# Performance work log

Hardware: AMD Instinct MI355X
Metric: run time of the kernel (lower is better)

Reference implementation:

```python
import jax, jax.numpy as jnp
import numpy as np

B, SQ, SK, D, UNITS = 4, 2048, 2048, 1024, 1024

def setup_inputs() -> dict:
    key = jax.random.key(0)
    ks = jax.random.split(key, 5)
    scale = 1.0 / np.sqrt(D)
    return {
        "q": jax.random.normal(ks[0], (B, SQ, D), dtype=jnp.float32),
        "k": jax.random.normal(ks[1], (B, SK, D), dtype=jnp.float32),
        "v": jax.random.normal(ks[2], (B, SK, D), dtype=jnp.float32),
        "W1_w": jax.random.normal(ks[3], (D, UNITS), dtype=jnp.float32) * scale,
        "W1_b": jnp.zeros((UNITS,), dtype=jnp.float32),
        "W2_w": jax.random.normal(ks[4], (D, UNITS), dtype=jnp.float32) * scale,
        "W2_b": jnp.zeros((UNITS,), dtype=jnp.float32),
    }

def reference(q, k, v, W1_w, W1_b, W2_w, W2_b):
    # Dense projections (keras Dense: x @ W + b)
    l1 = q @ W1_w + W1_b            # [B, Sq, units]
    l2 = k @ W2_w + W2_b            # [B, Sk, units]
    # score = l1 @ l2^T, scaled by sqrt(score.shape[2]) == sqrt(Sk) (as in original)
    inv_scale = 1.0 / np.sqrt(k.shape[1]).astype(np.float32)
    score = jnp.einsum('bqu,bku->bqk', l1, l2) * inv_scale  # [B, Sq, Sk]
    dist = jax.nn.softmax(score, axis=-1)
    att = jnp.einsum('bqk,bkd->bqd', dist, v)               # [B, Sq, d_v]
    return att
```

## Files before the change

### kernel.cpp

```cpp
#include <hip/hip_runtime.h>
#include <cmath>
#include <stdint.h>


typedef short short8 __attribute__((ext_vector_type(8)));
typedef float f32x4 __attribute__((ext_vector_type(4)));
typedef __bf16 bf16x8 __attribute__((ext_vector_type(8)));
typedef unsigned int u32x4 __attribute__((ext_vector_type(4)));

typedef __attribute__((address_space(3))) void lds_void;
typedef __attribute__((address_space(1))) void gbl_void;

__device__ __forceinline__ unsigned short f2b(float x) {
    unsigned u = __builtin_bit_cast(unsigned, x);
    u += 0x7fffu + ((u >> 16) & 1u);
    return (unsigned short)(u >> 16);
}

__global__ void prep_kernel(const float* __restrict__ v,
                            const float* __restrict__ W1,
                            const float* __restrict__ W2,
                            unsigned short* __restrict__ vT,
                            unsigned short* __restrict__ W1t,
                            unsigned short* __restrict__ W2t,
                            float* __restrict__ rs) {
    const int bz = blockIdx.z;
    const int t = threadIdx.x;
    const int tid2 = blockIdx.y * 64 + blockIdx.x;

    if (bz == 4 && tid2 >= 256 && tid2 < 288) {
        if (rs) rs[(tid2 - 256) * 256 + t] = 0.f;
        return;
    }

    __shared__ float tile[64][65];
    const float* in;
    unsigned short* out;
    int R, C;
    if (bz < 4) {
        R = 2048; C = 1024;
        in = v + (long)bz * R * C;
        out = vT + (long)bz * R * C;
    } else {
        R = 1024; C = 1024;
        if (tid2 >= 256) return;
        in = (bz == 4) ? W1 : W2;
        out = (bz == 4) ? W1t : W2t;
    }
    const int rt = (tid2 >> 4) * 64;
    const int ct = (tid2 & 15) * 64;

    {
        const int rr = t >> 2;
        const int cb = (t & 3) * 16;
        const float* src = in + (long)(rt + rr) * C + ct + cb;
#pragma unroll
        for (int u = 0; u < 4; u++) {
            float4 a = *(const float4*)(src + 4 * u);
            tile[rr][cb + 4 * u + 0] = a.x;
            tile[rr][cb + 4 * u + 1] = a.y;
            tile[rr][cb + 4 * u + 2] = a.z;
            tile[rr][cb + 4 * u + 3] = a.w;
        }
    }
    __syncthreads();
    {
        const int cc = t >> 2;
        const int rb = (t & 3) * 16;
        unsigned short* dst = out + (long)(ct + cc) * R + rt + rb;
#pragma unroll
        for (int u = 0; u < 2; u++) {
            union { short8 v8; unsigned short us[8]; } o;
#pragma unroll
            for (int e = 0; e < 8; e++) o.us[e] = f2b(tile[rb + 8 * u + e][cc]);
            *(short8*)(dst + 8 * u) = o.v8;
        }
    }
}

__device__ __forceinline__ void load16_to_lds(const unsigned short* g,
                                              unsigned short* l) {
    __builtin_amdgcn_global_load_lds((gbl_void*)g, (lds_void*)l, 16, 0, 0);
}

template <int MODE, int CASTA>
__global__ __launch_bounds__(512, 4) void gemm256_kernel(
                               const unsigned short* __restrict__ A,
                               const unsigned short* __restrict__ Bt,
                               const float* __restrict__ bias0,
                               const float* __restrict__ bias1,
                               float* __restrict__ rowsum,
                               void* __restrict__ Cout,
                               int M, int N, int K,
                               float scale,
                               long sA, long sB, long sC,
                               const float* __restrict__ Afq,
                               const float* __restrict__ Afk) {
    __shared__ __align__(16) unsigned short As[256 * 64];
    __shared__ __align__(16) unsigned short Bs[128 * 64];

    int bx, by, bz;
    {
        const int nx = gridDim.x;
        const int Rt = gridDim.y * gridDim.z;
        if ((Rt & 7) == 0) {
            int flat = ((int)blockIdx.z * gridDim.y + blockIdx.y) * nx + blockIdx.x;
            int rpx = Rt >> 3;
            int c = flat & 7;
            int j = flat >> 3;
            bx = j / rpx;
            int yg = c * rpx + (j - bx * rpx);
            bz = yg / gridDim.y;
            by = yg - bz * gridDim.y;
        } else {
            bx = blockIdx.x; by = blockIdx.y; bz = blockIdx.z;
        }
    }

    Bt += (long)bz * sB;

    const int t = threadIdx.x;
    const int lane = t & 63;
    const int wave = t >> 6;
    const int wm = wave >> 1, wn = wave & 1;
    const int row0 = by * 256;
    const int col0 = bx * 128;

    const int rS = lane >> 3;
    const int kOffS = ((lane & 7) ^ rS) * 8;
    const unsigned short* gA[4];
    const float* fA[4];
    unsigned short* lA[4];
    const unsigned short* gB[2];
    unsigned short* lB[2];
#pragma unroll
    for (int i = 0; i < 4; i++) {
        const int rowl = wave * 32 + i * 8;
        lA[i] = As + rowl * 64;
        if (CASTA) {
            const float* Af = bz ? Afk : Afq;
            fA[i] = Af + (long)(row0 + rowl + rS) * K + kOffS;
        } else {
            gA[i] = A + (long)bz * sA + (long)(row0 + rowl + rS) * K + kOffS;
        }
    }
#pragma unroll
    for (int i = 0; i < 2; i++) {
        const int rowl = wave * 16 + i * 8;
        gB[i] = Bt + (long)(col0 + rowl + rS) * K + kOffS;
        lB[i] = Bs + rowl * 64;
    }

    const int lr = lane & 15;
    const int quad = lane >> 4;
    const int pc0 = (quad ^ (lr & 7)) * 8;
    const int pc1 = ((4 + quad) ^ (lr & 7)) * 8;

    f32x4 acc[4][4];
#pragma unroll
    for (int i = 0; i < 4; i++)
#pragma unroll
        for (int j = 0; j < 4; j++) acc[i][j] = f32x4{0.f, 0.f, 0.f, 0.f};

    for (int k0 = 0; k0 < K; k0 += 64) {
#pragma unroll
        for (int i = 0; i < 2; i++) load16_to_lds(gB[i] + k0, lB[i]);
        if (CASTA) {
#pragma unroll
            for (int i = 0; i < 4; i++) {
                const float* s = fA[i] + k0;
                float4 x = *(const float4*)(s);
                float4 y = *(const float4*)(s + 4);
                unsigned w0, w1, w2, w3;
                asm("v_cvt_pk_bf16_f32 %0, %1, %2" : "=v"(w0) : "v"(x.x), "v"(x.y));
                asm("v_cvt_pk_bf16_f32 %0, %1, %2" : "=v"(w1) : "v"(x.z), "v"(x.w));
                asm("v_cvt_pk_bf16_f32 %0, %1, %2" : "=v"(w2) : "v"(y.x), "v"(y.y));
                asm("v_cvt_pk_bf16_f32 %0, %1, %2" : "=v"(w3) : "v"(y.z), "v"(y.w));
                *(u32x4*)(lA[i] + lane * 8) = u32x4{w0, w1, w2, w3};
            }
        } else {
#pragma unroll
            for (int i = 0; i < 4; i++) load16_to_lds(gA[i] + k0, lA[i]);
        }
        __syncthreads();

#pragma unroll
        for (int ks = 0; ks < 2; ks++) {
            const int pc = ks ? pc1 : pc0;
            bf16x8 a[4], b[4];
#pragma unroll
            for (int i = 0; i < 4; i++) {
                a[i] = __builtin_bit_cast(bf16x8,
                    *(const short8*)(As + (wm * 64 + i * 16 + lr) * 64 + pc));
                b[i] = __builtin_bit_cast(bf16x8,
                    *(const short8*)(Bs + (wn * 64 + i * 16 + lr) * 64 + pc));
            }
#pragma unroll
            for (int i = 0; i < 4; i++)
#pragma unroll
                for (int j = 0; j < 4; j++)
                    acc[i][j] = __builtin_amdgcn_mfma_f32_16x16x32_bf16(
                        a[i], b[j], acc[i][j], 0, 0, 0);
        }
        __syncthreads();
    }

    const long cbase = (long)bz * sC;

    if (MODE == 0) {
        const float* bp = (bz && bias1) ? bias1 : bias0;
#pragma unroll
        for (int j = 0; j < 4; j++) {
            const int gcol = col0 + wn * 64 + j * 16 + lr;
            const float bv = bp[gcol];
#pragma unroll
            for (int i = 0; i < 4; i++) {
                const int growb = row0 + wm * 64 + i * 16 + quad * 4;
#pragma unroll
                for (int r = 0; r < 4; r++) {
                    float val = acc[i][j][r] * scale + bv;
                    ((unsigned short*)Cout)[cbase + (long)(growb + r) * N + gcol] = f2b(val);
                }
            }
        }
    } else {
        float psum[4][4];
#pragma unroll
        for (int i = 0; i < 4; i++)
#pragma unroll
            for (int r = 0; r < 4; r++) psum[i][r] = 0.f;
#pragma unroll
        for (int j = 0; j < 4; j++) {
            const int gcol = col0 + wn * 64 + j * 16 + lr;
#pragma unroll
            for (int i = 0; i < 4; i++) {
                const int growb = row0 + wm * 64 + i * 16 + quad * 4;
#pragma unroll
                for (int r = 0; r < 4; r++) {
                    float e = __expf(acc[i][j][r] * scale);
                    psum[i][r] += e;
                    ((unsigned short*)Cout)[cbase + (long)(growb + r) * N + gcol] = f2b(e);
                }
            }
        }
#pragma unroll
        for (int i = 0; i < 4; i++)
#pragma unroll
            for (int r = 0; r < 4; r++) {
                float s = psum[i][r];
                s += __shfl_xor(s, 1);
                s += __shfl_xor(s, 2);
                s += __shfl_xor(s, 4);
                s += __shfl_xor(s, 8);
                if (lr == 0) {
                    const int grow = row0 + wm * 64 + i * 16 + quad * 4 + r;
                    atomicAdd(rowsum + (long)bz * M + grow, s);
                }
            }
    }
}

template <int MODE>
__global__ void gemm128_kernel(const unsigned short* __restrict__ A,
                               const unsigned short* __restrict__ Bt,
                               const float* __restrict__ bias0,
                               const float* __restrict__ bias1,
                               float* __restrict__ rowsum,
                               void* __restrict__ Cout,
                               int M, int N, int K,
                               float scale,
                               long sA, long sB, long sC) {
    __shared__ __align__(16) unsigned short As[128 * 64];
    __shared__ __align__(16) unsigned short Bs[128 * 64];

    int bx, by, bz;
    {
        const int nx = gridDim.x;
        const int Rt = gridDim.y * gridDim.z;
        if ((Rt & 7) == 0) {
            int flat = ((int)blockIdx.z * gridDim.y + blockIdx.y) * nx + blockIdx.x;
            int rpx = Rt >> 3;
            int c = flat & 7;
            int j = flat >> 3;
            bx = j / rpx;
            int yg = c * rpx + (j - bx * rpx);
            bz = yg / gridDim.y;
            by = yg - bz * gridDim.y;
        } else {
            bx = blockIdx.x; by = blockIdx.y; bz = blockIdx.z;
        }
    }

    A  += (long)bz * sA;
    Bt += (long)bz * sB;

    const int t = threadIdx.x;
    const int lane = t & 63;
    const int wave = t >> 6;
    const int wm = wave >> 1, wn = wave & 1;
    const int row0 = by * 128;
    const int col0 = bx * 128;

    const int rS = lane >> 3;
    const int kOffS = ((lane & 7) ^ rS) * 8;
    const unsigned short* gA[4];
    const unsigned short* gB[4];
    unsigned short* lA[4];
    unsigned short* lB[4];
#pragma unroll
    for (int i = 0; i < 4; i++) {
        const int rowl = i * 32 + wave * 8 + rS;
        const int ldsrow = i * 32 + wave * 8;
        gA[i] = A  + (long)(row0 + rowl) * K + kOffS;
        gB[i] = Bt + (long)(col0 + rowl) * K + kOffS;
        lA[i] = As + ldsrow * 64;
        lB[i] = Bs + ldsrow * 64;
    }

    const int lr = lane & 15;
    const int quad = lane >> 4;
    const int pc0 = (quad ^ (lr & 7)) * 8;
    const int pc1 = ((4 + quad) ^ (lr & 7)) * 8;

    f32x4 acc[4][4];
#pragma unroll
    for (int i = 0; i < 4; i++)
#pragma unroll
        for (int j = 0; j < 4; j++) acc[i][j] = f32x4{0.f, 0.f, 0.f, 0.f};

    for (int k0 = 0; k0 < K; k0 += 64) {
#pragma unroll
        for (int i = 0; i < 4; i++) {
            load16_to_lds(gA[i] + k0, lA[i]);
            load16_to_lds(gB[i] + k0, lB[i]);
        }
        __syncthreads();

#pragma unroll
        for (int ks = 0; ks < 2; ks++) {
            const int pc = ks ? pc1 : pc0;
            bf16x8 a[4], b[4];
#pragma unroll
            for (int i = 0; i < 4; i++) {
                a[i] = __builtin_bit_cast(bf16x8,
                    *(const short8*)(As + (wm * 64 + i * 16 + lr) * 64 + pc));
                b[i] = __builtin_bit_cast(bf16x8,
                    *(const short8*)(Bs + (wn * 64 + i * 16 + lr) * 64 + pc));
            }
#pragma unroll
            for (int i = 0; i < 4; i++)
#pragma unroll
                for (int j = 0; j < 4; j++)
                    acc[i][j] = __builtin_amdgcn_mfma_f32_16x16x32_bf16(
                        a[i], b[j], acc[i][j], 0, 0, 0);
        }
        __syncthreads();
    }

    const long cbase = (long)bz * sC;

    if (MODE == 2) {
#pragma unroll
        for (int i = 0; i < 4; i++) {
            const int growb = row0 + wm * 64 + i * 16 + quad * 4;
#pragma unroll
            for (int r = 0; r < 4; r++) {
                const float inv = 1.0f / rowsum[(long)bz * M + growb + r];
#pragma unroll
                for (int j = 0; j < 4; j++) {
                    const int gcol = col0 + wn * 64 + j * 16 + lr;
                    ((float*)Cout)[cbase + (long)(growb + r) * N + gcol] =
                        acc[i][j][r] * inv;
                }
            }
        }
    }
}

extern "C" void kernel_launch(void* const* d_in, const int* in_sizes, int n_in,
                              void* d_out, int out_size, void* d_ws, size_t ws_size,
                              hipStream_t stream) {
    const float* q   = (const float*)d_in[0];
    const float* k   = (const float*)d_in[1];
    const float* v   = (const float*)d_in[2];
    const float* W1w = (const float*)d_in[3];
    const float* W1b = (const float*)d_in[4];
    const float* W2w = (const float*)d_in[5];
    const float* W2b = (const float*)d_in[6];
    float* out = (float*)d_out;

    const int B = 4, SQ = 2048, SK = 2048, D = 1024, U = 1024;
    char* ws = (char*)d_ws;
    const size_t MB = 1024 * 1024;
    unsigned short* vT  = (unsigned short*)(ws + 32 * MB);
    unsigned short* W1t = (unsigned short*)(ws + 48 * MB);
    unsigned short* W2t = (unsigned short*)(ws + 50 * MB);
    unsigned short* l1  = (unsigned short*)(ws + 52 * MB);
    unsigned short* l2  = (unsigned short*)(ws + 68 * MB);
    unsigned short* sc  = (unsigned short*)(ws + 0);

    float* rowsum;
    bool prep_zeroes_rowsum;
    if (ws_size >= 85 * MB) {
        rowsum = (float*)(ws + 84 * MB);
        prep_zeroes_rowsum = true;
    } else {
        rowsum = (float*)(ws + 50 * MB);
        prep_zeroes_rowsum = false;
    }

    prep_kernel<<<dim3(64, 8, 6), 256, 0, stream>>>(
        v, W1w, W2w, vT, W1t, W2t,
        prep_zeroes_rowsum ? rowsum : nullptr);
    gemm256_kernel<0, 1><<<dim3(U / 128, (B * SQ) / 256, 2), 512, 0, stream>>>(
        nullptr, W1t, W1b, W2b, nullptr, l1, B * SQ, U, D, 1.0f,
        0, (long)1024 * 1024, (long)8 * 1024 * 1024, q, k);
    if (!prep_zeroes_rowsum)
        hipMemsetAsync(rowsum, 0, (size_t)B * SQ * sizeof(float), stream);
    const float invs = 1.0f / sqrtf((float)SK);
    gemm256_kernel<1, 0><<<dim3(SK / 128, SQ / 256, B), 512, 0, stream>>>(
        l1, l2, nullptr, nullptr, rowsum, sc, SQ, SK, U, invs,
        (long)SQ * U, (long)SK * U, (long)SQ * SK, nullptr, nullptr);
    gemm128_kernel<2><<<dim3(D / 128, SQ / 128, B), 256, 0, stream>>>(
        sc, vT, nullptr, nullptr, rowsum, out, SQ, D, SK, 1.0f,
        (long)SQ * SK, (long)D * SK, (long)SQ * D);
}
```

Baseline: 261.7 us.

## Pre-cast q/k to bf16 in prep and fold V transpose into score GEMM

The fp32-to-bf16 conversion of q and k moves out of the projection GEMM's inner loop into the prep kernel, so the projection GEMM can stream both operands with async global_load_lds. The V transpose-and-cast leaves the prep kernel and runs as extra blocks (bz >= 4) of the score GEMM launch, so it overlaps with score tiles instead of running as a separate pass. The trade-off is extra HBM traffic for the bf16 copies of q and k, and the transpose blocks now compete with GEMM blocks for the CUs.

```diff
diff --git a/kernel.cpp b/kernel.cpp
--- a/kernel.cpp
+++ b/kernel.cpp
@@ -6,7 +6,6 @@
 typedef short short8 __attribute__((ext_vector_type(8)));
 typedef float f32x4 __attribute__((ext_vector_type(4)));
 typedef __bf16 bf16x8 __attribute__((ext_vector_type(8)));
-typedef unsigned int u32x4 __attribute__((ext_vector_type(4)));
 
 typedef __attribute__((address_space(3))) void lds_void;
 typedef __attribute__((address_space(1))) void gbl_void;
@@ -17,36 +16,45 @@
     return (unsigned short)(u >> 16);
 }
 
-__global__ void prep_kernel(const float* __restrict__ v,
+__global__ void prep_kernel(const float* __restrict__ q,
+                            const float* __restrict__ k,
                             const float* __restrict__ W1,
                             const float* __restrict__ W2,
-                            unsigned short* __restrict__ vT,
+                            unsigned short* __restrict__ qbf,
+                            unsigned short* __restrict__ kbf,
                             unsigned short* __restrict__ W1t,
                             unsigned short* __restrict__ W2t,
                             float* __restrict__ rs) {
     const int bz = blockIdx.z;
     const int t = threadIdx.x;
+
+    if (bz >= 2) {
+        const float* in = (bz < 4) ? q : k;
+        unsigned short* out = (bz < 4) ? qbf : kbf;
+        const long zi = (bz - 2) & 1;
+        const long fb = zi * 2048 + blockIdx.y * 64 + blockIdx.x;
+        const long i = (fb * 256 + t) * 8;
+        float4 a = *(const float4*)(in + i);
+        float4 b = *(const float4*)(in + i + 4);
+        union { short8 v8; unsigned short u[8]; } r;
+        r.u[0] = f2b(a.x); r.u[1] = f2b(a.y); r.u[2] = f2b(a.z); r.u[3] = f2b(a.w);
+        r.u[4] = f2b(b.x); r.u[5] = f2b(b.y); r.u[6] = f2b(b.z); r.u[7] = f2b(b.w);
+        *(short8*)(out + i) = r.v8;
+        return;
+    }
+
     const int tid2 = blockIdx.y * 64 + blockIdx.x;
 
-    if (bz == 4 && tid2 >= 256 && tid2 < 288) {
+    if (bz == 0 && tid2 >= 256 && tid2 < 288) {
         if (rs) rs[(tid2 - 256) * 256 + t] = 0.f;
         return;
     }
+    if (tid2 >= 256) return;
 
     __shared__ float tile[64][65];
-    const float* in;
-    unsigned short* out;
-    int R, C;
-    if (bz < 4) {
-        R = 2048; C = 1024;
-        in = v + (long)bz * R * C;
-        out = vT + (long)bz * R * C;
-    } else {
-        R = 1024; C = 1024;
-        if (tid2 >= 256) return;
-        in = (bz == 4) ? W1 : W2;
-        out = (bz == 4) ? W1t : W2t;
-    }
+    const float* in = (bz == 0) ? W1 : W2;
+    unsigned short* out = (bz == 0) ? W1t : W2t;
+    const int C = 1024, R = 1024;
     const int rt = (tid2 >> 4) * 64;
     const int ct = (tid2 & 15) * 64;
 
@@ -83,7 +91,7 @@
     __builtin_amdgcn_global_load_lds((gbl_void*)g, (lds_void*)l, 16, 0, 0);
 }
 
-template <int MODE, int CASTA>
+template <int MODE>
 __global__ __launch_bounds__(512, 4) void gemm256_kernel(
                                const unsigned short* __restrict__ A,
                                const unsigned short* __restrict__ Bt,
@@ -94,8 +102,8 @@
                                int M, int N, int K,
                                float scale,
                                long sA, long sB, long sC,
-                               const float* __restrict__ Afq,
-                               const float* __restrict__ Afk) {
+                               const float* __restrict__ Vsrc,
+                               unsigned short* __restrict__ VTdst) {
     __shared__ __align__(16) unsigned short As[256 * 64];
     __shared__ __align__(16) unsigned short Bs[128 * 64];
 
@@ -117,9 +125,52 @@
         }
     }
 
+    const int t = threadIdx.x;
+
+    if (MODE == 1 && bz >= 4) {
+        const int half = t >> 8;
+        const int st = t & 255;
+        const int ti2 = (((bz - 4) * (int)gridDim.y + by) * (int)gridDim.x + bx) * 2 + half;
+        const int batch = ti2 >> 9;
+        const int ti = ti2 & 511;
+        const int rt = (ti >> 4) * 64;
+        const int ct = (ti & 15) * 64;
+        const float* in = Vsrc + (long)batch * 2048 * 1024;
+        unsigned short* outp = VTdst + (long)batch * 1024 * 2048;
+        unsigned short* tile = As + half * 8192;
+        {
+            const int rr = st >> 2;
+            const int cb = (st & 3) * 16;
+            const float* src = in + (long)(rt + rr) * 1024 + ct + cb;
+            unsigned short* trow = tile + rr * 65 + cb;
+#pragma unroll
+            for (int u = 0; u < 4; u++) {
+                float4 a = *(const float4*)(src + 4 * u);
+                trow[4 * u + 0] = f2b(a.x);
+                trow[4 * u + 1] = f2b(a.y);
+                trow[4 * u + 2] = f2b(a.z);
+                trow[4 * u + 3] = f2b(a.w);
+            }
+        }
+        __syncthreads();
+        {
+            const int cc = st >> 2;
+            const int rb = (st & 3) * 16;
+            unsigned short* dst = outp + (long)(ct + cc) * 2048 + rt + rb;
+#pragma unroll
+            for (int u = 0; u < 2; u++) {
+                union { short8 v8; unsigned short us[8]; } o;
+#pragma unroll
+                for (int e = 0; e < 8; e++) o.us[e] = tile[(rb + 8 * u + e) * 65 + cc];
+                *(short8*)(dst + 8 * u) = o.v8;
+            }
+        }
+        return;
+    }
+
+    A  += (long)bz * sA;
     Bt += (long)bz * sB;
 
-    const int t = threadIdx.x;
     const int lane = t & 63;
     const int wave = t >> 6;
     const int wm = wave >> 1, wn = wave & 1;
@@ -129,20 +180,14 @@
     const int rS = lane >> 3;
     const int kOffS = ((lane & 7) ^ rS) * 8;
     const unsigned short* gA[4];
-    const float* fA[4];
     unsigned short* lA[4];
     const unsigned short* gB[2];
     unsigned short* lB[2];
 #pragma unroll
     for (int i = 0; i < 4; i++) {
         const int rowl = wave * 32 + i * 8;
+        gA[i] = A + (long)(row0 + rowl + rS) * K + kOffS;
         lA[i] = As + rowl * 64;
-        if (CASTA) {
-            const float* Af = bz ? Afk : Afq;
-            fA[i] = Af + (long)(row0 + rowl + rS) * K + kOffS;
-        } else {
-            gA[i] = A + (long)bz * sA + (long)(row0 + rowl + rS) * K + kOffS;
-        }
     }
 #pragma unroll
     for (int i = 0; i < 2; i++) {
@@ -164,24 +209,9 @@
 
     for (int k0 = 0; k0 < K; k0 += 64) {
 #pragma unroll
+        for (int i = 0; i < 4; i++) load16_to_lds(gA[i] + k0, lA[i]);
+#pragma unroll
         for (int i = 0; i < 2; i++) load16_to_lds(gB[i] + k0, lB[i]);
-        if (CASTA) {
-#pragma unroll
-            for (int i = 0; i < 4; i++) {
-                const float* s = fA[i] + k0;
-                float4 x = *(const float4*)(s);
-                float4 y = *(const float4*)(s + 4);
-                unsigned w0, w1, w2, w3;
-                asm("v_cvt_pk_bf16_f32 %0, %1, %2" : "=v"(w0) : "v"(x.x), "v"(x.y));
-                asm("v_cvt_pk_bf16_f32 %0, %1, %2" : "=v"(w1) : "v"(x.z), "v"(x.w));
-                asm("v_cvt_pk_bf16_f32 %0, %1, %2" : "=v"(w2) : "v"(y.x), "v"(y.y));
-                asm("v_cvt_pk_bf16_f32 %0, %1, %2" : "=v"(w3) : "v"(y.z), "v"(y.w));
-                *(u32x4*)(lA[i] + lane * 8) = u32x4{w0, w1, w2, w3};
-            }
-        } else {
-#pragma unroll
-            for (int i = 0; i < 4; i++) load16_to_lds(gA[i] + k0, lA[i]);
-        }
         __syncthreads();
 
 #pragma unroll
@@ -263,12 +293,9 @@
 template <int MODE>
 __global__ void gemm128_kernel(const unsigned short* __restrict__ A,
                                const unsigned short* __restrict__ Bt,
-                               const float* __restrict__ bias0,
-                               const float* __restrict__ bias1,
                                float* __restrict__ rowsum,
                                void* __restrict__ Cout,
                                int M, int N, int K,
-                               float scale,
                                long sA, long sB, long sC) {
     __shared__ __align__(16) unsigned short As[128 * 64];
     __shared__ __align__(16) unsigned short Bs[128 * 64];
@@ -392,6 +419,8 @@
     const int B = 4, SQ = 2048, SK = 2048, D = 1024, U = 1024;
     char* ws = (char*)d_ws;
     const size_t MB = 1024 * 1024;
+    unsigned short* qbf = (unsigned short*)(ws + 0);
+    unsigned short* kbf = (unsigned short*)(ws + 16 * MB);
     unsigned short* vT  = (unsigned short*)(ws + 32 * MB);
     unsigned short* W1t = (unsigned short*)(ws + 48 * MB);
     unsigned short* W2t = (unsigned short*)(ws + 50 * MB);
@@ -409,19 +438,20 @@
         prep_zeroes_rowsum = false;
     }
 
-    prep_kernel<<<dim3(64, 8, 6), 256, 0, stream>>>(
-        v, W1w, W2w, vT, W1t, W2t,
+    prep_kernel<<<dim3(64, 32, 6), 256, 0, stream>>>(
+        q, k, W1w, W2w, qbf, kbf, W1t, W2t,
         prep_zeroes_rowsum ? rowsum : nullptr);
-    gemm256_kernel<0, 1><<<dim3(U / 128, (B * SQ) / 256, 2), 512, 0, stream>>>(
-        nullptr, W1t, W1b, W2b, nullptr, l1, B * SQ, U, D, 1.0f,
-        0, (long)1024 * 1024, (long)8 * 1024 * 1024, q, k);
+    gemm256_kernel<0><<<dim3(U / 128, (B * SQ) / 256, 2), 512, 0, stream>>>(
+        qbf, W1t, W1b, W2b, nullptr, l1, B * SQ, U, D, 1.0f,
+        (long)8 * 1024 * 1024, (long)1024 * 1024, (long)8 * 1024 * 1024,
+        nullptr, nullptr);
     if (!prep_zeroes_rowsum)
         hipMemsetAsync(rowsum, 0, (size_t)B * SQ * sizeof(float), stream);
     const float invs = 1.0f / sqrtf((float)SK);
-    gemm256_kernel<1, 0><<<dim3(SK / 128, SQ / 256, B), 512, 0, stream>>>(
+    gemm256_kernel<1><<<dim3(SK / 128, SQ / 256, B + 8), 512, 0, stream>>>(
         l1, l2, nullptr, nullptr, rowsum, sc, SQ, SK, U, invs,
-        (long)SQ * U, (long)SK * U, (long)SQ * SK, nullptr, nullptr);
+        (long)SQ * U, (long)SK * U, (long)SQ * SK, v, vT);
     gemm128_kernel<2><<<dim3(D / 128, SQ / 128, B), 256, 0, stream>>>(
-        sc, vT, nullptr, nullptr, rowsum, out, SQ, D, SK, 1.0f,
+        sc, vT, rowsum, out, SQ, D, SK,
         (long)SQ * SK, (long)D * SK, (long)SQ * D);
 }
```

New measurement: 327.6 us. +25.2%, slower.
